# Kernel tuning notes

Measured on AMD Instinct MI355X. Metric: run time of the kernel, lower is better.

## Reference

```python
import jax, jax.numpy as jnp
import numpy as np

N = 50000      # nodes
E = 160000     # edges
NFEAT = 1024
NHID = 512
NCLASS = 64


def _unif(k, shape, fan):
    s = 1.0 / np.sqrt(fan)
    return jax.random.uniform(k, shape, jnp.float32, -s, s)


def setup_inputs() -> dict:
    key = jax.random.key(0)
    ks = jax.random.split(key, 16)
    x = jax.random.normal(ks[0], (N, NFEAT), jnp.float32)
    adj_row = jax.random.randint(ks[1], (E,), 0, N, jnp.int32)
    adj_col = jax.random.randint(ks[2], (E,), 0, N, jnp.int32)
    adj_val = jax.random.uniform(ks[3], (E,), jnp.float32)
    # gc1: nfeat -> nhid (stdv = 1/sqrt(out_features))
    W1 = _unif(ks[4], (NFEAT, NHID), NHID)
    b1 = _unif(ks[5], (NHID,), NHID)
    # residual projection for gc1 (nn.Linear nfeat->nhid)
    p1W = _unif(ks[6], (NFEAT, NHID), NFEAT)
    p1b = _unif(ks[7], (NHID,), NFEAT)
    # gc3: nhid -> nhid (shared across 4 applications)
    W3 = _unif(ks[8], (NHID, NHID), NHID)
    b3 = _unif(ks[9], (NHID,), NHID)
    # gc2: nhid -> nclass
    W2 = _unif(ks[10], (NHID, NCLASS), NCLASS)
    b2 = _unif(ks[11], (NCLASS,), NCLASS)
    # residual projection for gc2 (nn.Linear nhid->nclass)
    p2W = _unif(ks[12], (NHID, NCLASS), NHID)
    p2b = _unif(ks[13], (NCLASS,), NHID)
    return {"x": x, "adj_row": adj_row, "adj_col": adj_col, "adj_val": adj_val,
            "W1": W1, "b1": b1, "p1W": p1W, "p1b": p1b,
            "W3": W3, "b3": b3, "W2": W2, "b2": b2, "p2W": p2W, "p2b": p2b}


def _spmm(row, col, val, support):
    # out[i] = sum_e val[e] * support[col[e]] for row[e] == i   (adj @ support)
    return jax.ops.segment_sum(val[:, None] * support[col], row, num_segments=N)


def reference(x, adj_row, adj_col, adj_val, W1, b1, p1W, p1b, W3, b3, W2, b2, p2W, p2b):
    def gc_proj(inp, W, b, pW, pb):
        # shapes differ -> projected residual
        out = _spmm(adj_row, adj_col, adj_val, inp @ W) + b
        return jax.nn.relu(out + inp @ pW + pb)

    def gc_res(inp, W, b):
        # same shape -> identity residual
        out = _spmm(adj_row, adj_col, adj_val, inp @ W) + b
        return jax.nn.relu(out + inp)

    h = jax.nn.relu(gc_proj(x, W1, b1, p1W, p1b))       # [N, NHID]
    for _ in range(4):                                   # gc3 shared weights x4
        h = jax.nn.relu(gc_res(h, W3, b3))
    h = gc_proj(h, W2, b2, p2W, p2b)                     # [N, NCLASS]
    return jax.nn.log_softmax(h, axis=1)
```

## Files before the change

### kernel.cpp

```cpp
#include <hip/hip_runtime.h>

typedef __attribute__((ext_vector_type(8))) short bf16x8;
typedef __attribute__((ext_vector_type(8))) unsigned short ushort8;
typedef __attribute__((ext_vector_type(4))) float f32x4;

#define NNODES 50000
#define NEDGES 160000
#define MP     50176
#define NB_SCAN 196

__device__ __forceinline__ float bf2f(unsigned short u) {
  return __uint_as_float(((unsigned int)u) << 16);
}
__device__ __forceinline__ unsigned short f2bf(float f) {
  unsigned int u = __float_as_uint(f);
  u += 0x7fffu + ((u >> 16) & 1u);
  return (unsigned short)(u >> 16);
}
__device__ __forceinline__ void gld16(const void* g, void* l) {
  __builtin_amdgcn_global_load_lds((__attribute__((address_space(1))) void*)g,
                                   (__attribute__((address_space(3))) void*)l, 16, 0, 0);
}

__global__ void k_hist(const int* __restrict__ row, int* __restrict__ cnt, int n) {
  int i = blockIdx.x * 256 + threadIdx.x;
  if (i < n) atomicAdd(&cnt[row[i]], 1);
}

__global__ void k_block_reduce(const int* __restrict__ cnt, int* __restrict__ bsum, int n) {
  __shared__ int sd[256];
  int i = blockIdx.x * 256 + threadIdx.x;
  sd[threadIdx.x] = (i < n) ? cnt[i] : 0;
  __syncthreads();
  for (int o = 128; o > 0; o >>= 1) {
    if (threadIdx.x < o) sd[threadIdx.x] += sd[threadIdx.x + o];
    __syncthreads();
  }
  if (threadIdx.x == 0) bsum[blockIdx.x] = sd[0];
}

__global__ void k_scan_bsum(const int* __restrict__ bsum, int* __restrict__ boff, int nb,
                            int* __restrict__ rowptr, int n, int E) {
  __shared__ int sd[256];
  int v = (threadIdx.x < nb) ? bsum[threadIdx.x] : 0;
  sd[threadIdx.x] = v;
  __syncthreads();
  for (int o = 1; o < 256; o <<= 1) {
    int t = (threadIdx.x >= o) ? sd[threadIdx.x - o] : 0;
    __syncthreads();
    sd[threadIdx.x] += t;
    __syncthreads();
  }
  if (threadIdx.x < nb) boff[threadIdx.x] = sd[threadIdx.x] - v;
  if (threadIdx.x == 0) rowptr[n] = E;
}

__global__ void k_block_scan(const int* __restrict__ cnt, const int* __restrict__ boff,
                             int* __restrict__ rowptr, int* __restrict__ cursor, int n) {
  __shared__ int sd[256];
  int i = blockIdx.x * 256 + threadIdx.x;
  int v = (i < n) ? cnt[i] : 0;
  sd[threadIdx.x] = v;
  __syncthreads();
  for (int o = 1; o < 256; o <<= 1) {
    int t = (threadIdx.x >= o) ? sd[threadIdx.x - o] : 0;
    __syncthreads();
    sd[threadIdx.x] += t;
    __syncthreads();
  }
  if (i < n) {
    int r = boff[blockIdx.x] + sd[threadIdx.x] - v;
    rowptr[i] = r;
    cursor[i] = r;
  }
}

__global__ void k_scatter(const int* __restrict__ row, const int* __restrict__ col,
                          const float* __restrict__ val, int* __restrict__ cursor,
                          int* __restrict__ scol, float* __restrict__ sval, int n) {
  int e = blockIdx.x * 256 + threadIdx.x;
  if (e < n) {
    int p = atomicAdd(&cursor[row[e]], 1);
    scol[p] = col[e];
    sval[p] = val[e];
  }
}

__global__ void k_cast_x(const float* __restrict__ x, unsigned short* __restrict__ xb, int nRealRows) {
  size_t idx = ((size_t)blockIdx.x * 256 + threadIdx.x) * 8;
  if (idx >= (size_t)MP * 1024) return;
  int row = (int)(idx >> 10);
  ushort8 o;
  if (row < nRealRows) {
    float4 a = *(const float4*)(x + idx);
    float4 b = *(const float4*)(x + idx + 4);
    o[0] = f2bf(a.x); o[1] = f2bf(a.y); o[2] = f2bf(a.z); o[3] = f2bf(a.w);
    o[4] = f2bf(b.x); o[5] = f2bf(b.y); o[6] = f2bf(b.z); o[7] = f2bf(b.w);
  } else {
    o = (ushort8){0,0,0,0,0,0,0,0};
  }
  *(ushort8*)(xb + idx) = o;
}

__global__ void k_pack_all(const float* __restrict__ W1, const float* __restrict__ p1W,
                           const float* __restrict__ W3, const float* __restrict__ W2,
                           const float* __restrict__ p2W,
                           const float* __restrict__ b1, const float* __restrict__ p1b,
                           const float* __restrict__ b2, const float* __restrict__ p2b,
                           unsigned short* __restrict__ B1t, unsigned short* __restrict__ W3t,
                           unsigned short* __restrict__ B2t,
                           float* __restrict__ bias1, float* __restrict__ bias2) {
  int z = blockIdx.z;
  int tx = threadIdx.x, ty = threadIdx.y;
  if (z == 5) {
    if (blockIdx.x || blockIdx.y) return;
    int t = ty * 32 + tx;
    bias1[t] = b1[t] + p1b[t];
    bias1[t + 256] = b1[t + 256] + p1b[t + 256];
    if (t < 64) bias2[t] = b2[t] + p2b[t];
    return;
  }
  const float* src; unsigned short* dst; int K, srcW, nc, dstOff;
  if (z == 0)      { src = W1;  dst = B1t; K = 1024; srcW = 512; nc = 512; dstOff = 0; }
  else if (z == 1) { src = p1W; dst = B1t; K = 1024; srcW = 512; nc = 512; dstOff = 512; }
  else if (z == 2) { src = W3;  dst = W3t; K = 512;  srcW = 512; nc = 512; dstOff = 0; }
  else if (z == 3) { src = W2;  dst = B2t; K = 512;  srcW = 64;  nc = 64;  dstOff = 0; }
  else             { src = p2W; dst = B2t; K = 512;  srcW = 64;  nc = 64;  dstOff = 64; }
  int k0 = blockIdx.x * 32, n0 = blockIdx.y * 32;
  if (k0 >= K || n0 >= nc) return;
  __shared__ float tile[32][33];
  for (int i = ty; i < 32; i += 8)
    tile[i][tx] = src[(size_t)(k0 + i) * srcW + (n0 + tx)];
  __syncthreads();
  for (int i = ty; i < 32; i += 8)
    dst[(size_t)(dstOff + n0 + i) * K + (k0 + tx)] = f2bf(tile[tx][i]);
}

__global__ __launch_bounds__(256, 4) void k_gemm128(
    const unsigned short* __restrict__ A, const unsigned short* __restrict__ Bt,
    unsigned short* __restrict__ C, int M, int N, int K) {
  extern __shared__ char smem[];
  const int NT = N >> 7;
  const int nwg = gridDim.x;
  const int q = nwg >> 3, r = nwg & 7;
  const int xcd = blockIdx.x & 7, local = blockIdx.x >> 3;
  const int swz = (xcd < r ? xcd * (q + 1) : r * (q + 1) + (xcd - r) * q) + local;
  const int mt = swz / NT, nt = swz % NT;

  const int tid = threadIdx.x;
  const int w = tid >> 6, lane = tid & 63;
  const int wr = w >> 1, wc = w & 1;

  const int srow = tid >> 2;
  const int schunk = (tid & 3) ^ ((srow >> 1) & 3);
  const unsigned short* gA = A + (size_t)(mt * 128 + srow) * K + schunk * 8;
  const unsigned short* gB = Bt + (size_t)(nt * 128 + srow) * K + schunk * 8;
  const size_t rs64 = (size_t)64 * K;
  const int wb = w << 10;

  const int l15 = lane & 15;
  const int cpos = ((lane >> 4) ^ ((l15 >> 1) & 3)) << 4;
  const int aOff = (wr * 64 + l15) * 64 + cpos;
  const int bOff = 8192 + (wc * 64 + l15) * 64 + cpos;

  f32x4 acc[4][4] = {};
  const int T = K >> 5;

  auto STAGE = [&](int t) {
    char* db = smem + (t % 3) * 16384 + wb;
    const unsigned short* a = gA + t * 32;
    const unsigned short* b = gB + t * 32;
    gld16(a, db);
    gld16(a + rs64, db + 4096);
    gld16(b, db + 8192);
    gld16(b + rs64, db + 12288);
  };

  STAGE(0); STAGE(1);

  for (int t = 0; t < T; ++t) {
    if (t < T - 1) asm volatile("s_waitcnt vmcnt(4)" ::: "memory");
    else           asm volatile("s_waitcnt vmcnt(0)" ::: "memory");
    __builtin_amdgcn_s_barrier();
    __builtin_amdgcn_sched_barrier(0);
    if (t + 2 < T) STAGE(t + 2);
    const int bb = (t % 3) * 16384;
    bf16x8 af[4];
#pragma unroll
    for (int m = 0; m < 4; ++m) af[m] = *(const bf16x8*)(smem + bb + aOff + m * 1024);
    __builtin_amdgcn_s_setprio(1);
#pragma unroll
    for (int n = 0; n < 4; ++n) {
      bf16x8 bfr = *(const bf16x8*)(smem + bb + bOff + n * 1024);
#pragma unroll
      for (int m = 0; m < 4; ++m)
        acc[m][n] = __builtin_amdgcn_mfma_f32_16x16x32_bf16(af[m], bfr, acc[m][n], 0, 0, 0);
    }
    __builtin_amdgcn_s_setprio(0);
  }

  const int r0 = mt * 128 + wr * 64 + (lane >> 4) * 4;
  const int c0e = nt * 128 + wc * 64 + l15;
#pragma unroll
  for (int m = 0; m < 4; ++m)
#pragma unroll
    for (int n = 0; n < 4; ++n)
#pragma unroll
      for (int j = 0; j < 4; ++j)
        C[(size_t)(r0 + m * 16 + j) * N + (c0e + n * 16)] = f2bf(acc[m][n][j]);
}

__global__ __launch_bounds__(256) void k_spmm_ep512(
    const int* __restrict__ rowptr, const int* __restrict__ scol, const float* __restrict__ sval,
    const unsigned short* __restrict__ s, int sStride,
    const unsigned short* __restrict__ res, int resStride,
    const float* __restrict__ bias,
    unsigned short* __restrict__ o, int oStride, int nReal, int nTot) {
  int gw = (blockIdx.x * 256 + threadIdx.x) >> 6;
  int lane = threadIdx.x & 63;
  if (gw >= nTot) return;
  unsigned short* op = o + (size_t)gw * oStride + lane * 8;
  if (gw >= nReal) {
    *(ushort8*)op = (ushort8){0,0,0,0,0,0,0,0};
    return;
  }
  float acc[8] = {0.f,0.f,0.f,0.f,0.f,0.f,0.f,0.f};
  int e0 = rowptr[gw], e1 = rowptr[gw + 1];
  int e = e0;
  for (; e + 2 <= e1; e += 2) {
    int c0 = scol[e], c1 = scol[e + 1];
    float v0 = sval[e], v1 = sval[e + 1];
    ushort8 s0 = *(const ushort8*)(s + (size_t)c0 * sStride + lane * 8);
    ushort8 s1 = *(const ushort8*)(s + (size_t)c1 * sStride + lane * 8);
#pragma unroll
    for (int k = 0; k < 8; ++k) acc[k] += v0 * bf2f(s0[k]) + v1 * bf2f(s1[k]);
  }
  if (e < e1) {
    int c = scol[e];
    float v = sval[e];
    ushort8 sv = *(const ushort8*)(s + (size_t)c * sStride + lane * 8);
#pragma unroll
    for (int k = 0; k < 8; ++k) acc[k] += v * bf2f(sv[k]);
  }
  ushort8 rv = *(const ushort8*)(res + (size_t)gw * resStride + lane * 8);
  ushort8 ov;
#pragma unroll
  for (int k = 0; k < 8; ++k) {
    float tt = acc[k] + bias[lane * 8 + k] + bf2f(rv[k]);
    ov[k] = f2bf(fmaxf(tt, 0.f));
  }
  *(ushort8*)op = ov;
}

__global__ __launch_bounds__(256) void k_spmm_lsm(
    const int* __restrict__ rowptr, const int* __restrict__ scol, const float* __restrict__ sval,
    const unsigned short* __restrict__ g2, const float* __restrict__ bias2,
    float* __restrict__ out, int n) {
  int gw = (blockIdx.x * 256 + threadIdx.x) >> 6;
  int lane = threadIdx.x & 63;
  if (gw >= n) return;
  int e0 = rowptr[gw], e1 = rowptr[gw + 1];
  float acc = 0.f;
  for (int e = e0; e < e1; ++e) {
    int c = scol[e];
    acc += sval[e] * bf2f(g2[(size_t)c * 128 + lane]);
  }
  float t = acc + bias2[lane] + bf2f(g2[(size_t)gw * 128 + 64 + lane]);
  float v = fmaxf(t, 0.f);
  float m = v;
#pragma unroll
  for (int o = 32; o > 0; o >>= 1) m = fmaxf(m, __shfl_xor(m, o));
  float ex = __expf(v - m);
  float ss = ex;
#pragma unroll
  for (int o = 32; o > 0; o >>= 1) ss += __shfl_xor(ss, o);
  out[(size_t)gw * 64 + lane] = v - m - __logf(ss);
}

extern "C" void kernel_launch(void* const* d_in, const int* in_sizes, int n_in,
                              void* d_out, int out_size, void* d_ws, size_t ws_size,
                              hipStream_t stream) {
  const float* x    = (const float*)d_in[0];
  const int*   arow = (const int*)d_in[1];
  const int*   acol = (const int*)d_in[2];
  const float* aval = (const float*)d_in[3];
  const float* W1   = (const float*)d_in[4];
  const float* b1   = (const float*)d_in[5];
  const float* p1W  = (const float*)d_in[6];
  const float* p1b  = (const float*)d_in[7];
  const float* W3   = (const float*)d_in[8];
  const float* b3   = (const float*)d_in[9];
  const float* W2   = (const float*)d_in[10];
  const float* b2   = (const float*)d_in[11];
  const float* p2W  = (const float*)d_in[12];
  const float* p2b  = (const float*)d_in[13];
  float* out = (float*)d_out;

  char* wsp = (char*)d_ws;
  size_t off = 0;
  auto take = [&](size_t bytes) -> char* {
    char* p = wsp + off;
    off = (off + bytes + 255) & ~(size_t)255;
    return p;
  };
  unsigned short* xb  = (unsigned short*)take((size_t)MP * 1024 * 2);
  unsigned short* g1  = (unsigned short*)take((size_t)MP * 1024 * 2);
  unsigned short* B1t = (unsigned short*)take((size_t)1024 * 1024 * 2);
  unsigned short* W3t = (unsigned short*)take((size_t)512 * 512 * 2);
  unsigned short* B2t = (unsigned short*)take((size_t)128 * 512 * 2);
  float* bias1 = (float*)take(512 * 4);
  float* bias2 = (float*)take(64 * 4);
  int*   cnt    = (int*)take((size_t)NNODES * 4);
  int*   rowptr = (int*)take((size_t)(NNODES + 1) * 4);
  int*   bsum   = (int*)take(256 * 4);
  int*   boff   = (int*)take(256 * 4);
  int*   scol   = (int*)take((size_t)NEDGES * 4);
  float* sval   = (float*)take((size_t)NEDGES * 4);
  unsigned short* h  = xb;
  unsigned short* s  = g1;
  unsigned short* g2 = g1;

  hipMemsetAsync(cnt, 0, (size_t)NNODES * 4, stream);
  k_hist<<<(NEDGES + 255) / 256, 256, 0, stream>>>(arow, cnt, NEDGES);
  k_block_reduce<<<NB_SCAN, 256, 0, stream>>>(cnt, bsum, NNODES);
  k_scan_bsum<<<1, 256, 0, stream>>>(bsum, boff, NB_SCAN, rowptr, NNODES, NEDGES);
  k_block_scan<<<NB_SCAN, 256, 0, stream>>>(cnt, boff, rowptr, cnt, NNODES);
  k_scatter<<<(NEDGES + 255) / 256, 256, 0, stream>>>(arow, acol, aval, cnt, scol, sval, NEDGES);

  k_cast_x<<<(int)(((size_t)MP * 1024 / 8 + 255) / 256), 256, 0, stream>>>(x, xb, NNODES);
  k_pack_all<<<dim3(32, 16, 6), dim3(32, 8), 0, stream>>>(W1, p1W, W3, W2, p2W,
                                                          b1, p1b, b2, p2b,
                                                          B1t, W3t, B2t, bias1, bias2);

  k_gemm128<<<392 * 8, 256, 49152, stream>>>(xb, B1t, g1, MP, 1024, 1024);
  k_spmm_ep512<<<MP / 4, 256, 0, stream>>>(rowptr, scol, sval, g1, 1024, g1 + 512, 1024,
                                           bias1, h, 512, NNODES, MP);
  for (int i = 0; i < 4; ++i) {
    k_gemm128<<<392 * 4, 256, 49152, stream>>>(h, W3t, s, MP, 512, 512);
    k_spmm_ep512<<<MP / 4, 256, 0, stream>>>(rowptr, scol, sval, s, 512, h, 512,
                                             b3, h, 512, NNODES, MP);
  }
  k_gemm128<<<392, 256, 49152, stream>>>(h, B2t, g2, MP, 128, 512);
  k_spmm_lsm<<<(NNODES + 3) / 4, 256, 0, stream>>>(rowptr, scol, sval, g2, bias2, out, NNODES);
}
```

Baseline: 605.9 us.

## Add 128x256 GEMM tile for first layer and unroll SpMM edge loops

Adds a 512-thread GEMM kernel with a 128x256 output tile and a three-stage LDS pipeline, and uses it for the large first-layer GEMM (K=1024, N=1024). The wider tile raises reuse of the A operand per byte loaded. The SpMM epilogue kernel now gathers four edges per iteration, and the log-softmax SpMM gathers two, to keep more loads in flight. The bigger tile uses more LDS (72KB) and likely more registers, which may lower occupancy.

```diff
diff --git a/kernel.cpp b/kernel.cpp
--- a/kernel.cpp
+++ b/kernel.cpp
@@ -136,6 +136,79 @@
     dst[(size_t)(dstOff + n0 + i) * K + (k0 + tx)] = f2bf(tile[tx][i]);
 }
 
+__global__ __launch_bounds__(512, 4) void k_gemm128x256(
+    const unsigned short* __restrict__ A, const unsigned short* __restrict__ Bt,
+    unsigned short* __restrict__ C, int M, int N, int K) {
+  extern __shared__ char smem[];
+  const int NT = N >> 8;
+  const int nwg = gridDim.x;
+  const int q = nwg >> 3, r = nwg & 7;
+  const int xcd = blockIdx.x & 7, local = blockIdx.x >> 3;
+  const int swz = (xcd < r ? xcd * (q + 1) : r * (q + 1) + (xcd - r) * q) + local;
+  const int mt = swz / NT, nt = swz % NT;
+
+  const int tid = threadIdx.x;
+  const int w = tid >> 6, lane = tid & 63;
+  const int wr = w >> 2, wc = w & 3;
+
+  const int srow = tid >> 2;
+  const int schunk = (tid & 3) ^ ((tid >> 3) & 3);
+  const unsigned short* gA = A + (size_t)(mt * 128 + srow) * K + schunk * 8;
+  const unsigned short* gB = Bt + (size_t)(nt * 256 + srow) * K + schunk * 8;
+  const size_t rs128 = (size_t)128 * K;
+  const int wb = w << 10;
+
+  const int l15 = lane & 15;
+  const int cpos = ((lane >> 4) ^ ((l15 >> 1) & 3)) << 4;
+  const int aOff = (wr * 64 + l15) * 64 + cpos;
+  const int bOff = 8192 + (wc * 64 + l15) * 64 + cpos;
+
+  f32x4 acc[4][4] = {};
+  const int T = K >> 5;
+
+  auto STAGE = [&](int t) {
+    char* db = smem + (t % 3) * 24576 + wb;
+    const unsigned short* a = gA + t * 32;
+    const unsigned short* b = gB + t * 32;
+    gld16(a, db);
+    gld16(b, db + 8192);
+    gld16(b + rs128, db + 16384);
+  };
+
+  STAGE(0); STAGE(1);
+
+  for (int t = 0; t < T; ++t) {
+    if (t < T - 1) asm volatile("s_waitcnt vmcnt(3)" ::: "memory");
+    else           asm volatile("s_waitcnt vmcnt(0)" ::: "memory");
+    __builtin_amdgcn_s_barrier();
+    __builtin_amdgcn_sched_barrier(0);
+    if (t + 2 < T) STAGE(t + 2);
+    const int bb = (t % 3) * 24576;
+    bf16x8 af[4];
+#pragma unroll
+    for (int m = 0; m < 4; ++m) af[m] = *(const bf16x8*)(smem + bb + aOff + m * 1024);
+    __builtin_amdgcn_s_setprio(1);
+#pragma unroll
+    for (int n = 0; n < 4; ++n) {
+      bf16x8 bfr = *(const bf16x8*)(smem + bb + bOff + n * 1024);
+#pragma unroll
+      for (int m = 0; m < 4; ++m)
+        acc[m][n] = __builtin_amdgcn_mfma_f32_16x16x32_bf16(af[m], bfr, acc[m][n], 0, 0, 0);
+    }
+    __builtin_amdgcn_s_setprio(0);
+  }
+
+  const int r0 = mt * 128 + wr * 64 + (lane >> 4) * 4;
+  const int c0e = nt * 256 + wc * 64 + l15;
+#pragma unroll
+  for (int m = 0; m < 4; ++m)
+#pragma unroll
+    for (int n = 0; n < 4; ++n)
+#pragma unroll
+      for (int j = 0; j < 4; ++j)
+        C[(size_t)(r0 + m * 16 + j) * N + (c0e + n * 16)] = f2bf(acc[m][n][j]);
+}
+
 __global__ __launch_bounds__(256, 4) void k_gemm128(
     const unsigned short* __restrict__ A, const unsigned short* __restrict__ Bt,
     unsigned short* __restrict__ C, int M, int N, int K) {
@@ -227,13 +300,25 @@
   float acc[8] = {0.f,0.f,0.f,0.f,0.f,0.f,0.f,0.f};
   int e0 = rowptr[gw], e1 = rowptr[gw + 1];
   int e = e0;
-  for (; e + 2 <= e1; e += 2) {
+  for (; e + 4 <= e1; e += 4) {
+    int c0 = scol[e], c1 = scol[e + 1], c2 = scol[e + 2], c3 = scol[e + 3];
+    float v0 = sval[e], v1 = sval[e + 1], v2 = sval[e + 2], v3 = sval[e + 3];
+    ushort8 s0 = *(const ushort8*)(s + (size_t)c0 * sStride + lane * 8);
+    ushort8 s1 = *(const ushort8*)(s + (size_t)c1 * sStride + lane * 8);
+    ushort8 s2 = *(const ushort8*)(s + (size_t)c2 * sStride + lane * 8);
+    ushort8 s3 = *(const ushort8*)(s + (size_t)c3 * sStride + lane * 8);
+#pragma unroll
+    for (int k = 0; k < 8; ++k)
+      acc[k] += v0 * bf2f(s0[k]) + v1 * bf2f(s1[k]) + v2 * bf2f(s2[k]) + v3 * bf2f(s3[k]);
+  }
+  if (e + 2 <= e1) {
     int c0 = scol[e], c1 = scol[e + 1];
     float v0 = sval[e], v1 = sval[e + 1];
     ushort8 s0 = *(const ushort8*)(s + (size_t)c0 * sStride + lane * 8);
     ushort8 s1 = *(const ushort8*)(s + (size_t)c1 * sStride + lane * 8);
 #pragma unroll
     for (int k = 0; k < 8; ++k) acc[k] += v0 * bf2f(s0[k]) + v1 * bf2f(s1[k]);
+    e += 2;
   }
   if (e < e1) {
     int c = scol[e];
@@ -261,10 +346,15 @@
   if (gw >= n) return;
   int e0 = rowptr[gw], e1 = rowptr[gw + 1];
   float acc = 0.f;
-  for (int e = e0; e < e1; ++e) {
-    int c = scol[e];
-    acc += sval[e] * bf2f(g2[(size_t)c * 128 + lane]);
-  }
+  int e = e0;
+  for (; e + 2 <= e1; e += 2) {
+    int c0 = scol[e], c1 = scol[e + 1];
+    float v0 = sval[e], v1 = sval[e + 1];
+    float a0 = bf2f(g2[(size_t)c0 * 128 + lane]);
+    float a1 = bf2f(g2[(size_t)c1 * 128 + lane]);
+    acc += v0 * a0 + v1 * a1;
+  }
+  if (e < e1) acc += sval[e] * bf2f(g2[(size_t)scol[e] * 128 + lane]);
   float t = acc + bias2[lane] + bf2f(g2[(size_t)gw * 128 + 64 + lane]);
   float v = fmaxf(t, 0.f);
   float m = v;
@@ -332,7 +422,7 @@
                                                           b1, p1b, b2, p2b,
                                                           B1t, W3t, B2t, bias1, bias2);
 
-  k_gemm128<<<392 * 8, 256, 49152, stream>>>(xb, B1t, g1, MP, 1024, 1024);
+  k_gemm128x256<<<392 * 4, 512, 73728, stream>>>(xb, B1t, g1, MP, 1024, 1024);
   k_spmm_ep512<<<MP / 4, 256, 0, stream>>>(rowptr, scol, sval, g1, 1024, g1 + 512, 1024,
                                            bias1, h, 512, NNODES, MP);
   for (int i = 0; i < 4; ++i) {
```

Measured after the change: 583.6 us. 3.7% less time.
